# Kernel optimization log

Hardware: AMD Instinct MI355X
Metric: run time of the kernel (lower is better)

The kernel has to match this reference:

```python
import jax, jax.numpy as jnp
import numpy as np
from jax import lax

N, L, B = 256, 20, 10      # batch, max_seq (baskets), max_bas (items/basket)
D, H, ASP, K = 128, 128, 4, 16  # dim, h, aspects, nbNUM
NITEMS = 20000
H2 = 2 * H


def setup_inputs() -> dict:
    key = jax.random.key(0)
    ks = jax.random.split(key, 20)
    nrm = lambda k, shape, s=0.05: (jax.random.normal(k, shape) * s).astype(jnp.float32)
    seq = jax.random.randint(ks[0], (N, L, B), 0, NITEMS + 1)          # indices into itemEmb
    uHis = jax.random.uniform(ks[1], (N, NITEMS), dtype=jnp.float32)   # dense user history
    itemEmb = nrm(ks[2], (NITEMS + 1, D), 0.1).at[0].set(0.0)          # padding_idx=0 row zeroed
    fc1_w = nrm(ks[3], (1, L * B * D)); fc1_b = jnp.zeros((1,), jnp.float32)
    aspProju = nrm(ks[4], (ASP, 1, H))
    aspProji = nrm(ks[5], (ASP, D, H))
    dh_w = nrm(ks[6], (H, D)); dh_b = jnp.zeros((H,), jnp.float32)
    wih0 = nrm(ks[7], (4 * H2, H2)); whh0 = nrm(ks[8], (4 * H2, H2))
    bih0 = jnp.zeros((4 * H2,), jnp.float32); bhh0 = jnp.zeros((4 * H2,), jnp.float32)
    wih1 = nrm(ks[9], (4 * H2, H2)); whh1 = nrm(ks[10], (4 * H2, H2))
    bih1 = jnp.zeros((4 * H2,), jnp.float32); bhh1 = jnp.zeros((4 * H2,), jnp.float32)
    out_w = nrm(ks[11], (NITEMS, H2)); out_b = jnp.zeros((NITEMS,), jnp.float32)
    his_w = nrm(ks[12], (H2, NITEMS)); his_b = jnp.zeros((H2,), jnp.float32)
    g1_w = nrm(ks[13], (1, H2)); g1_b = jnp.zeros((1,), jnp.float32)
    g2_w = nrm(ks[14], (1, H2)); g2_b = jnp.zeros((1,), jnp.float32)
    return dict(seq=seq, uHis=uHis, itemEmb=itemEmb, fc1_w=fc1_w, fc1_b=fc1_b,
                aspProju=aspProju, aspProji=aspProji, dh_w=dh_w, dh_b=dh_b,
                wih0=wih0, whh0=whh0, bih0=bih0, bhh0=bhh0,
                wih1=wih1, whh1=whh1, bih1=bih1, bhh1=bhh1,
                out_w=out_w, out_b=out_b, his_w=his_w, his_b=his_b,
                g1_w=g1_w, g1_b=g1_b, g2_w=g2_w, g2_b=g2_b)


def _lstm_layer(x, wih, whh, bih, bhh):
    # x: [N, T, in]; PyTorch gate order i, f, g, o
    Hs = whh.shape[1]
    def step(carry, xt):
        h, c = carry
        g = xt @ wih.T + bih + h @ whh.T + bhh
        i, f, gg, o = jnp.split(g, 4, axis=-1)
        c = jax.nn.sigmoid(f) * c + jax.nn.sigmoid(i) * jnp.tanh(gg)
        h = jax.nn.sigmoid(o) * jnp.tanh(c)
        return (h, c), h
    h0 = jnp.zeros((x.shape[0], Hs), x.dtype)
    _, ys = lax.scan(step, (h0, h0), jnp.swapaxes(x, 0, 1))
    return jnp.swapaxes(ys, 0, 1)


def reference(seq, uHis, itemEmb, fc1_w, fc1_b, aspProju, aspProji, dh_w, dh_b,
              wih0, whh0, bih0, bhh0, wih1, whh1, bih1, bhh1,
              out_w, out_b, his_w, his_b, g1_w, g1_b, g2_w, g2_b):
    n, l, b = seq.shape
    embs = itemEmb[seq]                                   # [N,L,B,D]
    # MIE_user: fresh fc1 -> scalar per user, project per aspect
    u_embs = embs.reshape(n, -1) @ fc1_w.T + fc1_b        # [N,1]
    userAsp = jnp.tanh(jnp.einsum('no,aoh->nah', u_embs, aspProju))      # [N,ASP,H]
    # MIE_item
    itemAsp = jnp.tanh(jnp.einsum('nlbd,adh->nalbh', embs, aspProji))    # [N,ASP,L,B,H]
    # SNA: per-aspect exact L2 kNN over the batch (FAISS IndexFlatL2 equivalent)
    uA = jnp.transpose(jnp.tanh(userAsp), (1, 0, 2))      # [ASP,N,H] (double tanh, as in source)
    sq = jnp.sum(uA * uA, -1)                             # [ASP,N]
    dist = sq[:, :, None] + sq[:, None, :] - 2.0 * jnp.einsum('anh,amh->anm', uA, uA)
    dist = jnp.where(jnp.eye(n, dtype=bool)[None], -1.0, dist)   # self ranked first
    _, I = lax.top_k(lax.stop_gradient(-dist), K)         # [ASP,N,K] ascending distance
    I = I[:, :, 1:]                                       # drop self -> K-1 neighbors
    # sum of neighbor embeddings via multiplicity matmul (== gather+sum)
    M = jax.nn.one_hot(I, n, dtype=embs.dtype).sum(2)     # [ASP,N,N]
    nb_sum = jnp.einsum('apn,nlbd->aplbd', M, embs)       # [ASP,N,L,B,D]
    nb_h = nb_sum @ dh_w.T + dh_b                         # [ASP,N,L,B,H]
    embs_PI = jnp.transpose(nb_h.sum(axis=3), (1, 0, 2, 3))        # [N,ASP,L,H]
    embs_UI = jnp.tanh(itemAsp).sum(axis=3)               # [N,ASP,L,H] (double tanh)
    neighbAsps = jnp.concatenate([embs_UI, embs_PI], axis=-1)      # [N,ASP,L,2H]
    # raw view (not permute!) then max-pool over last dim of size ASP
    x = jnp.reshape(neighbAsps, (n, l, H2, ASP)).max(axis=-1)      # [N,L,2H]
    # 2-layer LSTM (eval mode: inter-layer dropout inactive)
    y = _lstm_layer(x, wih0, whh0, bih0, bhh0)
    y = _lstm_layer(y, wih1, whh1, bih1, bhh1)
    h_agg = jnp.tanh(y.sum(axis=1))                       # [N,2H]
    probs = jax.nn.softmax(h_agg @ out_w.T + out_b, axis=-1)       # [N,NITEMS]
    uHis_h = uHis @ his_w.T + his_b                        # [N,2H]
    gate = jax.nn.sigmoid(uHis_h @ g1_w.T + g1_b + h_agg @ g2_w.T + g2_b)  # [N,1]
    scores = gate * probs + (1.0 - gate) * uHis
    return scores
```

## Files before the change

kernel.cpp:

```cpp
#include <hip/hip_runtime.h>
#include <math.h>

#define N_ 256
#define L_ 20
#define B_ 10
#define D_ 128
#define H_ 128
#define ASP_ 4
#define KK_ 16
#define NIT_ 20000
#define H2_ 256
#define G4_ 1024
#define LBD_ 25600
#define NL_ 5120
#define NLB_ 51200

typedef __attribute__((ext_vector_type(8))) short bf16x8;
typedef __attribute__((ext_vector_type(4))) short bf16x4;
typedef __attribute__((ext_vector_type(4))) float f32x4;

__device__ __forceinline__ float sigf_fast(float x){
  return __builtin_amdgcn_rcpf(1.0f + __expf(-x));
}
__device__ __forceinline__ float tanh_fast(float x){
  return 1.0f - 2.0f*__builtin_amdgcn_rcpf(__expf(2.0f*x) + 1.0f);
}
__device__ __forceinline__ unsigned short f2b(float f){
  unsigned int u = __float_as_uint(f);
  unsigned int r = (u + 0x7FFFu + ((u>>16)&1u)) >> 16;
  return (unsigned short)r;
}
__device__ __forceinline__ float b2f(unsigned short b){
  return __uint_as_float(((unsigned int)b) << 16);
}

__global__ void k_gather(const int* __restrict__ seq, const float* __restrict__ itemEmb,
                         float* __restrict__ embs, unsigned short* __restrict__ ebh){
  int row = blockIdx.x;
  int t = threadIdx.x;
  int idx = seq[row];
  float v = itemEmb[idx*D_ + t];
  embs[row*D_ + t] = v;
  ebh[row*D_ + t] = f2b(v);
}

__global__ void k_fc1(const float* __restrict__ embs, const float* __restrict__ w,
                      const float* __restrict__ b, float* __restrict__ u){
  int n = blockIdx.x; int t = threadIdx.x;
  float s = 0.f;
  for (int i = t; i < LBD_; i += 256) s += embs[n*LBD_+i]*w[i];
  __shared__ float red[256];
  red[t]=s; __syncthreads();
  for (int o=128;o>0;o>>=1){ if(t<o) red[t]+=red[t+o]; __syncthreads(); }
  if(t==0) u[n]=red[0]+b[0];
}

__global__ void k_uasq(const float* __restrict__ u, const float* __restrict__ proju,
                       float* __restrict__ ua, float* __restrict__ sq){
  int an = blockIdx.x;
  int h = threadIdx.x;
  int a = an / N_, n = an % N_;
  float v = tanhf(tanhf(u[n]*proju[a*H_+h]));
  ua[an*H_ + h] = v;
  __shared__ float red[128];
  red[h] = v*v; __syncthreads();
  for(int o=64;o>0;o>>=1){ if(h<o) red[h]+=red[h+o]; __syncthreads(); }
  if(h==0) sq[an]=red[0];
}

__global__ __launch_bounds__(256) void k_disttopk(const float* __restrict__ ua,
    const float* __restrict__ sq, int* __restrict__ nbr){
  int n = blockIdx.x, a = blockIdx.y, m = threadIdx.x;
  __shared__ float un[H_];
  __shared__ float row[N_];
  if(m < H_) un[m] = ua[(a*N_+n)*H_ + m];
  __syncthreads();
  const float* um = &ua[(a*N_+m)*H_];
  float dot=0.f;
  for(int h=0;h<H_;h++) dot += un[h]*um[h];
  float dval = sq[a*N_+n] + sq[a*N_+m] - 2.f*dot;
  if(m==n) dval = -1.0f;
  row[m] = dval;
  __syncthreads();
  if(m < 64){
    int lane = m;
    int wid = a*N_+n;
    float v[4]; int idx[4];
    #pragma unroll
    for(int j=0;j<4;j++){ int mm = lane*4 + j; v[j] = row[mm]; idx[j] = mm; }
    for(int k=0;k<KK_;k++){
      float bv = v[0]; int bi = idx[0];
      #pragma unroll
      for(int j=1;j<4;j++)
        if(v[j] < bv || (v[j]==bv && idx[j] < bi)){ bv=v[j]; bi=idx[j]; }
      float rv = bv; int ri = bi;
      #pragma unroll
      for(int o=32;o>0;o>>=1){
        float ov = __shfl_xor(rv, o, 64);
        int   oi = __shfl_xor(ri, o, 64);
        if(ov < rv || (ov==rv && oi < ri)){ rv=ov; ri=oi; }
      }
      if((ri>>2) == lane){ v[ri&3] = 3.4e38f; idx[ri&3] = 0x7fffffff; }
      if(k>0 && lane==0) nbr[wid*(KK_-1)+(k-1)] = ri;
    }
  }
}

__global__ void k_eb(const float* __restrict__ embs, float* __restrict__ eb){
  int nl = blockIdx.x; int d = threadIdx.x;
  float s=0.f;
  const float* p = &embs[nl*B_*D_ + d];
  for(int b=0;b<B_;b++) s += p[b*D_];
  eb[nl*D_ + d] = s;
}

__global__ void k_prep(const float* __restrict__ wih0, const float* __restrict__ whh0,
                       const float* __restrict__ wih1, const float* __restrict__ whh1,
                       const float* __restrict__ bih0, const float* __restrict__ bhh0,
                       const float* __restrict__ bih1, const float* __restrict__ bhh1,
                       const float* __restrict__ proji,
                       float* __restrict__ wp0, unsigned short* __restrict__ whb0,
                       float* __restrict__ wp1, unsigned short* __restrict__ whb1,
                       float* __restrict__ bp0, float* __restrict__ bp1,
                       unsigned short* __restrict__ projb){
  int i = blockIdx.x*blockDim.x + threadIdx.x;
  if(i < 262144){
    int k=i%H2_, j=i/H2_, g=j/H2_, jj=j%H2_;
    wp0[(jj*4+g)*H2_+k] = wih0[i];
  } else if(i < 524288){
    int e=i-262144; int k=e%H2_, j=e/H2_, g=j/H2_, jj=j%H2_;
    whb0[(jj*4+g)*H2_+k] = f2b(whh0[e]);
  } else if(i < 786432){
    int e=i-524288; int k=e%H2_, j=e/H2_, g=j/H2_, jj=j%H2_;
    wp1[(jj*4+g)*H2_+k] = wih1[e];
  } else if(i < 1048576){
    int e=i-786432; int k=e%H2_, j=e/H2_, g=j/H2_, jj=j%H2_;
    whb1[(jj*4+g)*H2_+k] = f2b(whh1[e]);
  } else if(i < 1114112){
    int e=i-1048576; int h=e%H_, d=(e/H_)%D_, aa=e/(D_*H_);
    projb[(aa*H_+h)*D_+d] = f2b(proji[e]);
  } else if(i < 1115136){
    int j=i-1114112; int g=j/H2_, jj=j%H2_;
    bp0[jj*4+g] = bih0[j] + bhh0[j];
  } else if(i < 1116160){
    int j=i-1115136; int g=j/H2_, jj=j%H2_;
    bp1[jj*4+g] = bih1[j] + bhh1[j];
  }
}

__global__ __launch_bounds__(256) void k_uimm(const unsigned short* __restrict__ ebh,
                                              const unsigned short* __restrict__ projb,
                                              float* __restrict__ na){
  __shared__ char smem[53248];
  unsigned short* As = (unsigned short*)smem;
  unsigned short* Bs = (unsigned short*)(smem + 20480);
  float*          Cs = (float*)smem;

  int mb = blockIdx.x;
  int a  = blockIdx.y;
  int tid = threadIdx.x;

  const unsigned short* asrc = ebh + (size_t)mb*10240;
  #pragma unroll
  for(int t=0;t<5;t++){
    int c = tid + t*256;
    int row = c >> 4;
    *(bf16x8*)(As + 8*(c ^ (row&7))) = *(const bf16x8*)(asrc + 8*c);
  }
  const unsigned short* bsrc = projb + a*16384;
  #pragma unroll
  for(int t=0;t<8;t++){
    int c = tid + t*256;
    int row = c >> 4;
    *(bf16x8*)(Bs + 8*(c ^ (row&7))) = *(const bf16x8*)(bsrc + 8*c);
  }
  __syncthreads();

  int lane = tid & 63, wave = tid >> 6;
  int l15 = lane & 15, l4 = lane >> 4;
  f32x4 acc[5][2] = {};
  #pragma unroll
  for(int kk=0;kk<4;kk++){
    bf16x8 bfr[2];
    #pragma unroll
    for(int tc=0;tc<2;tc++){
      int h = (wave*2+tc)*16 + l15;
      int c = h*16 + kk*4 + l4;
      bfr[tc] = *(const bf16x8*)(Bs + 8*(c ^ (h&7)));
    }
    #pragma unroll
    for(int tr=0;tr<5;tr++){
      int R = tr*16 + l15;
      int c = R*16 + kk*4 + l4;
      bf16x8 afr = *(const bf16x8*)(As + 8*(c ^ (R&7)));
      acc[tr][0] = __builtin_amdgcn_mfma_f32_16x16x32_bf16(afr, bfr[0], acc[tr][0], 0,0,0);
      acc[tr][1] = __builtin_amdgcn_mfma_f32_16x16x32_bf16(afr, bfr[1], acc[tr][1], 0,0,0);
    }
  }
  __syncthreads();

  #pragma unroll
  for(int tr=0;tr<5;tr++)
    #pragma unroll
    for(int tc=0;tc<2;tc++){
      int col = (wave*2+tc)*16 + l15;
      #pragma unroll
      for(int r=0;r<4;r++){
        int R = tr*16 + l4*4 + r;
        Cs[R*128 + col] = tanh_fast(tanh_fast(acc[tr][tc][r]));
      }
    }
  __syncthreads();

  #pragma unroll
  for(int t=0;t<4;t++){
    int oi = t*256 + tid;
    int g = oi >> 7, col = oi & 127;
    float s = 0.f;
    const float* p = Cs + g*1280 + col;
    #pragma unroll
    for(int b=0;b<10;b++) s += p[b*128];
    int nl = mb*8 + g;
    int n = nl/L_, l = nl%L_;
    na[((size_t)(n*ASP_+a)*L_ + l)*H2_ + col] = s;
  }
}

__global__ __launch_bounds__(256) void k_uhismm(const float* __restrict__ U,
    const float* __restrict__ W, const float* __restrict__ bias, float* __restrict__ C){
  __shared__ unsigned short As[2048];
  __shared__ unsigned short Bs[2048];
  int tid = threadIdx.x;
  int m0 = blockIdx.y*64, n0 = blockIdx.x*64;
  int kb0 = blockIdx.z*800;
  int row = tid & 63, q = tid >> 6;
  int lane = tid & 63, wave = tid >> 6;
  int l15 = lane & 15, l4 = lane >> 4;
  int wr = (wave>>1)*32, wc = (wave&1)*32;
  f32x4 acc[2][2] = {};
  for(int s=0;s<25;s++){
    int k0 = kb0 + s*32 + q*8;
    {
      const float* pa = &U[(size_t)(m0+row)*NIT_ + k0];
      float4 a0 = *(const float4*)pa, a1 = *(const float4*)(pa+4);
      bf16x8 av;
      av[0]=f2b(a0.x); av[1]=f2b(a0.y); av[2]=f2b(a0.z); av[3]=f2b(a0.w);
      av[4]=f2b(a1.x); av[5]=f2b(a1.y); av[6]=f2b(a1.z); av[7]=f2b(a1.w);
      *(bf16x8*)(As + 8*tid) = av;
      const float* pb = &W[(size_t)(n0+row)*NIT_ + k0];
      float4 b0 = *(const float4*)pb, b1 = *(const float4*)(pb+4);
      bf16x8 bv;
      bv[0]=f2b(b0.x); bv[1]=f2b(b0.y); bv[2]=f2b(b0.z); bv[3]=f2b(b0.w);
      bv[4]=f2b(b1.x); bv[5]=f2b(b1.y); bv[6]=f2b(b1.z); bv[7]=f2b(b1.w);
      *(bf16x8*)(Bs + 8*tid) = bv;
    }
    __syncthreads();
    bf16x8 afr[2], bfr[2];
    #pragma unroll
    for(int mt=0;mt<2;mt++) afr[mt] = *(const bf16x8*)(As + 8*(l4*64 + wr + mt*16 + l15));
    #pragma unroll
    for(int nt=0;nt<2;nt++) bfr[nt] = *(const bf16x8*)(Bs + 8*(l4*64 + wc + nt*16 + l15));
    #pragma unroll
    for(int mt=0;mt<2;mt++)
      #pragma unroll
      for(int nt=0;nt<2;nt++)
        acc[mt][nt] = __builtin_amdgcn_mfma_f32_16x16x32_bf16(afr[mt], bfr[nt], acc[mt][nt], 0,0,0);
    __syncthreads();
  }
  #pragma unroll
  for(int mt=0;mt<2;mt++)
    #pragma unroll
    for(int nt=0;nt<2;nt++){
      int col = n0 + wc + nt*16 + l15;
      #pragma unroll
      for(int r=0;r<4;r++){
        int rw = m0 + wr + mt*16 + l4*4 + r;
        float v = acc[mt][nt][r];
        if(blockIdx.z==0) v += bias[col];
        atomicAdd(&C[rw*H2_ + col], v);
      }
    }
}

__global__ __launch_bounds__(256) void k_xgmm(const float* __restrict__ A_,
    const float* __restrict__ W, const float* __restrict__ bias,
    unsigned short* __restrict__ Cb){
  __shared__ unsigned short As[2048];
  __shared__ unsigned short Bs[2048];
  int tid = threadIdx.x;
  int n0 = blockIdx.x*64, m0 = blockIdx.y*64;
  int row = tid & 63, q = tid >> 6;
  int lane = tid & 63, wave = tid >> 6;
  int l15 = lane & 15, l4 = lane >> 4;
  int wr = (wave>>1)*32, wc = (wave&1)*32;
  f32x4 acc[2][2] = {};
  for(int s=0;s<8;s++){
    int k0 = s*32 + q*8;
    {
      const float* pa = &A_[(size_t)(m0+row)*H2_ + k0];
      float4 a0 = *(const float4*)pa, a1 = *(const float4*)(pa+4);
      bf16x8 av;
      av[0]=f2b(a0.x); av[1]=f2b(a0.y); av[2]=f2b(a0.z); av[3]=f2b(a0.w);
      av[4]=f2b(a1.x); av[5]=f2b(a1.y); av[6]=f2b(a1.z); av[7]=f2b(a1.w);
      *(bf16x8*)(As + 8*tid) = av;
      const float* pb = &W[(size_t)(n0+row)*H2_ + k0];
      float4 b0 = *(const float4*)pb, b1 = *(const float4*)(pb+4);
      bf16x8 bv;
      bv[0]=f2b(b0.x); bv[1]=f2b(b0.y); bv[2]=f2b(b0.z); bv[3]=f2b(b0.w);
      bv[4]=f2b(b1.x); bv[5]=f2b(b1.y); bv[6]=f2b(b1.z); bv[7]=f2b(b1.w);
      *(bf16x8*)(Bs + 8*tid) = bv;
    }
    __syncthreads();
    bf16x8 afr[2], bfr[2];
    #pragma unroll
    for(int mt=0;mt<2;mt++) afr[mt] = *(const bf16x8*)(As + 8*(l4*64 + wr + mt*16 + l15));
    #pragma unroll
    for(int nt=0;nt<2;nt++) bfr[nt] = *(const bf16x8*)(Bs + 8*(l4*64 + wc + nt*16 + l15));
    #pragma unroll
    for(int mt=0;mt<2;mt++)
      #pragma unroll
      for(int nt=0;nt<2;nt++)
        acc[mt][nt] = __builtin_amdgcn_mfma_f32_16x16x32_bf16(afr[mt], bfr[nt], acc[mt][nt], 0,0,0);
    __syncthreads();
  }
  #pragma unroll
  for(int mt=0;mt<2;mt++)
    #pragma unroll
    for(int nt=0;nt<2;nt++){
      int col = n0 + wc + nt*16 + l15;
      float bs = bias[col];
      #pragma unroll
      for(int r=0;r<4;r++){
        int rw = m0 + wr + mt*16 + l4*4 + r;
        Cb[(size_t)rw*G4_ + col] = f2b(acc[mt][nt][r] + bs);
      }
    }
}

__global__ void k_outb(const float* __restrict__ w, unsigned short* __restrict__ wb){
  int i = blockIdx.x*blockDim.x + threadIdx.x;
  const float* p = w + (size_t)i*8;
  float4 a = *(const float4*)p, b = *(const float4*)(p+4);
  bf16x8 v;
  v[0]=f2b(a.x); v[1]=f2b(a.y); v[2]=f2b(a.z); v[3]=f2b(a.w);
  v[4]=f2b(b.x); v[5]=f2b(b.y); v[6]=f2b(b.z); v[7]=f2b(b.w);
  *(bf16x8*)(wb + (size_t)i*8) = v;
}

__global__ __launch_bounds__(256) void k_logitsmm(const unsigned short* __restrict__ Ab,
    const unsigned short* __restrict__ Wb, const float* __restrict__ bias,
    float* __restrict__ C){
  int n0 = blockIdx.x*32;
  int tid = threadIdx.x;
  int lane = tid & 63, wave = tid >> 6;
  int l15 = lane & 15, l4 = lane >> 4;
  f32x4 acc[4][2] = {};
  #pragma unroll
  for(int kk=0;kk<8;kk++){
    int k0 = kk*32 + l4*8;
    bf16x8 bfr[2];
    #pragma unroll
    for(int nt=0;nt<2;nt++)
      bfr[nt] = *(const bf16x8*)(Wb + (size_t)(n0 + nt*16 + l15)*H2_ + k0);
    #pragma unroll
    for(int mt=0;mt<4;mt++){
      bf16x8 afr = *(const bf16x8*)(Ab + (size_t)(wave*64 + mt*16 + l15)*H2_ + k0);
      acc[mt][0] = __builtin_amdgcn_mfma_f32_16x16x32_bf16(afr, bfr[0], acc[mt][0], 0,0,0);
      acc[mt][1] = __builtin_amdgcn_mfma_f32_16x16x32_bf16(afr, bfr[1], acc[mt][1], 0,0,0);
    }
  }
  #pragma unroll
  for(int mt=0;mt<4;mt++)
    #pragma unroll
    for(int nt=0;nt<2;nt++){
      int col = n0 + nt*16 + l15;
      float bs = bias[col];
      #pragma unroll
      for(int r=0;r<4;r++){
        int row = wave*64 + mt*16 + l4*4 + r;
        C[(size_t)row*NIT_ + col] = acc[mt][nt][r] + bs;
      }
    }
}

__global__ __launch_bounds__(256) void k_gemm(const float* __restrict__ A, const float* __restrict__ W,
    float* __restrict__ C, const float* __restrict__ bias,
    int M, int Nn, int K, int kchunk, int atomic_mode){
  __shared__ float As[64][17];
  __shared__ float Ws[64][17];
  int tid = threadIdx.x;
  int tx = tid & 15, ty = tid >> 4;
  int m0 = blockIdx.y*64, n0 = blockIdx.x*64;
  int kb0 = blockIdx.z*kchunk;
  int kend = kb0 + kchunk; if(kend > K) kend = K;
  float acc[4][4] = {};
  int lrow = tid >> 2;
  int lc4 = (tid & 3) * 4;
  for(int kb = kb0; kb < kend; kb += 16){
    {
      int gr = m0 + lrow;
      float4 v = make_float4(0,0,0,0);
      if(gr < M) v = *(const float4*)&A[(long)gr*K + kb + lc4];
      As[lrow][lc4+0]=v.x; As[lrow][lc4+1]=v.y; As[lrow][lc4+2]=v.z; As[lrow][lc4+3]=v.w;
      int gw = n0 + lrow;
      float4 u = make_float4(0,0,0,0);
      if(gw < Nn) u = *(const float4*)&W[(long)gw*K + kb + lc4];
      Ws[lrow][lc4+0]=u.x; Ws[lrow][lc4+1]=u.y; Ws[lrow][lc4+2]=u.z; Ws[lrow][lc4+3]=u.w;
    }
    __syncthreads();
    for(int k=0;k<16;k++){
      float av[4], wv[4];
      #pragma unroll
      for(int r=0;r<4;r++) av[r]=As[ty*4+r][k];
      #pragma unroll
      for(int c=0;c<4;c++) wv[c]=Ws[tx*4+c][k];
      #pragma unroll
      for(int r=0;r<4;r++)
        #pragma unroll
        for(int c=0;c<4;c++) acc[r][c] += av[r]*wv[c];
    }
    __syncthreads();
  }
  for(int r=0;r<4;r++){
    int row = m0 + ty*4 + r; if(row >= M) continue;
    for(int c=0;c<4;c++){
      int col = n0 + tx*4 + c; if(col >= Nn) continue;
      float v = acc[r][c];
      if(bias && blockIdx.z==0) v += bias[col];
      if(atomic_mode) atomicAdd(&C[(long)row*Nn+col], v);
      else C[(long)row*Nn+col] = v;
    }
  }
}

__global__ void k_pi(const float* __restrict__ e2, const int* __restrict__ nbr,
                     const float* __restrict__ dh_b, float* __restrict__ na){
  int n = blockIdx.x, a = blockIdx.y, h = threadIdx.x;
  __shared__ int nb[KK_-1];
  if(h < KK_-1) nb[h] = nbr[(a*N_+n)*(KK_-1)+h];
  __syncthreads();
  float bias = (float)B_ * dh_b[h];
  for(int l=0;l<L_;l++){
    float s = bias;
    for(int k=0;k<KK_-1;k++) s += e2[(long)(nb[k]*L_ + l)*H_ + h];
    na[((long)(n*ASP_+a)*L_ + l)*H2_ + H_ + h] = s;
  }
}

__global__ void k_xmax(const float* __restrict__ na, float* __restrict__ x){
  int i = blockIdx.x*blockDim.x + threadIdx.x;
  if(i >= N_*L_*H2_) return;
  int n = i / (L_*H2_);
  int j = i % (L_*H2_);
  const float* p = &na[(long)n*ASP_*L_*H2_ + 4*j];
  x[i] = fmaxf(fmaxf(p[0],p[1]), fmaxf(p[2],p[3]));
}

__global__ __launch_bounds__(1024) void k_lstm_layer(
    const unsigned short* __restrict__ Whb,
    const unsigned short* __restrict__ xgb,
    float* __restrict__ Y){
  __shared__ unsigned short wc[65536];
  __shared__ unsigned short hs[2][16*H2_];
  int tid = threadIdx.x;
  int n0 = blockIdx.x * 16;
  int lane = tid & 63, wave = tid >> 6;
  int l15 = lane & 15, l4 = lane >> 4;
  int n = n0 + l15;
  float creg[4] = {0.f,0.f,0.f,0.f};
  {
    int ct0 = wave*4;
    #pragma unroll
    for(int it=0; it<8; it++){
      int c = it*64 + lane;
      int row = c >> 5;
      bf16x8 w8 = *(const bf16x8*)(Whb + (size_t)(ct0*16+row)*H2_ + (c&31)*8);
      *(bf16x8*)(wc + 8*((wave<<9) + (c ^ (row&7)))) = w8;
    }
  }
  const unsigned short* wptr[3];
  #pragma unroll
  for(int i=0;i<3;i++) wptr[i] = Whb + (size_t)((wave*4+1+i)*16 + l15)*H2_ + l4*8;
  const unsigned short* wc0 = wc + (wave<<12);
  __syncthreads();
  for(int t=0; t<L_; t++){
    bf16x4 xgv[4];
    #pragma unroll
    for(int i=0;i<4;i++){
      int jj = wave*16 + i*4 + l4;
      xgv[i] = *(const bf16x4*)(xgb + ((size_t)n*L_ + t)*G4_ + jj*4);
    }
    f32x4 acc[4] = {};
    if(t > 0){
      const unsigned short* hbuf = hs[(t+1)&1];
      bf16x8 hfr[8];
      #pragma unroll
      for(int kk=0; kk<8; kk++){
        int ch = l15*32 + kk*4 + l4;
        hfr[kk] = *(const bf16x8*)(hbuf + 8*(ch ^ (l15&7)));
      }
      #pragma unroll
      for(int kk=0; kk<8; kk++){
        bf16x8 wfr[4];
        wfr[0] = *(const bf16x8*)(wc0 + 8*((l15*32 + kk*4 + l4) ^ (l15&7)));
        #pragma unroll
        for(int i=0;i<3;i++) wfr[1+i] = *(const bf16x8*)(wptr[i] + kk*32);
        #pragma unroll
        for(int i=0;i<4;i++)
          acc[i] = __builtin_amdgcn_mfma_f32_16x16x32_bf16(wfr[i], hfr[kk], acc[i], 0,0,0);
      }
    }
    unsigned short* hout = hs[t&1];
    #pragma unroll
    for(int i=0;i<4;i++){
      int jj = wave*16 + i*4 + l4;
      float gi = acc[i][0] + b2f((unsigned short)xgv[i][0]);
      float gf = acc[i][1] + b2f((unsigned short)xgv[i][1]);
      float gg = acc[i][2] + b2f((unsigned short)xgv[i][2]);
      float go = acc[i][3] + b2f((unsigned short)xgv[i][3]);
      float cnew = sigf_fast(gf)*creg[i] + sigf_fast(gi)*tanh_fast(gg);
      creg[i] = cnew;
      float hnew = sigf_fast(go)*tanh_fast(cnew);
      Y[((size_t)n*L_ + t)*H2_ + jj] = hnew;
      int ch = l15*32 + (jj>>3);
      *(unsigned short*)((char*)hout + 16*(ch ^ (l15&7)) + (jj&7)*2) = f2b(hnew);
    }
    __syncthreads();
  }
}

__global__ void k_hagg_gate(const float* __restrict__ y1, const float* __restrict__ uhish,
                            const float* __restrict__ g1w, const float* __restrict__ g1b,
                            const float* __restrict__ g2w, const float* __restrict__ g2b,
                            float* __restrict__ hagg, unsigned short* __restrict__ haggb,
                            float* __restrict__ gate){
  int n = blockIdx.x; int jj = threadIdx.x;
  float s=0.f;
  for(int t=0;t<L_;t++) s += y1[((long)n*L_+t)*H2_ + jj];
  float v = tanhf(s);
  hagg[n*H2_+jj] = v;
  haggb[n*H2_+jj] = f2b(v);
  __shared__ float red[256];
  red[jj] = uhish[n*H2_+jj]*g1w[jj] + v*g2w[jj];
  __syncthreads();
  for(int o=128;o>0;o>>=1){ if(jj<o) red[jj]+=red[jj+o]; __syncthreads(); }
  if(jj==0) gate[n] = 1.f/(1.f+expf(-(red[0]+g1b[0]+g2b[0])));
}

__global__ __launch_bounds__(512) void k_softmax_out(const float* __restrict__ logits,
    const float* __restrict__ gate, const float* __restrict__ uHis, float* __restrict__ out){
  int n = blockIdx.x; int t = threadIdx.x;
  const float* row = &logits[(long)n*NIT_];
  float m = -3.4e38f;
  for(int i=t;i<NIT_;i+=512) m = fmaxf(m, row[i]);
  __shared__ float red[512];
  __shared__ float mm, ss;
  red[t]=m; __syncthreads();
  for(int o=256;o>0;o>>=1){ if(t<o) red[t]=fmaxf(red[t],red[t+o]); __syncthreads(); }
  if(t==0) mm = red[0];
  __syncthreads();
  float s=0.f;
  for(int i=t;i<NIT_;i+=512) s += __expf(row[i]-mm);
  __syncthreads();
  red[t]=s; __syncthreads();
  for(int o=256;o>0;o>>=1){ if(t<o) red[t]+=red[t+o]; __syncthreads(); }
  if(t==0) ss = red[0];
  __syncthreads();
  float g = gate[n];
  float* orow = out + (long)n*NIT_;
  const float* urow = uHis + (long)n*NIT_;
  for(int i=t;i<NIT_;i+=512){
    float p = __expf(row[i]-mm)/ss;
    orow[i] = g*p + (1.f-g)*urow[i];
  }
}

extern "C" void kernel_launch(void* const* d_in, const int* in_sizes, int n_in,
                              void* d_out, int out_size, void* d_ws, size_t ws_size,
                              hipStream_t stream) {
  const int*   seq     = (const int*)  d_in[0];
  const float* uHis    = (const float*)d_in[1];
  const float* itemEmb = (const float*)d_in[2];
  const float* fc1_w   = (const float*)d_in[3];
  const float* fc1_b   = (const float*)d_in[4];
  const float* aspProju= (const float*)d_in[5];
  const float* aspProji= (const float*)d_in[6];
  const float* dh_w    = (const float*)d_in[7];
  const float* dh_b    = (const float*)d_in[8];
  const float* wih0    = (const float*)d_in[9];
  const float* whh0    = (const float*)d_in[10];
  const float* bih0    = (const float*)d_in[11];
  const float* bhh0    = (const float*)d_in[12];
  const float* wih1    = (const float*)d_in[13];
  const float* whh1    = (const float*)d_in[14];
  const float* bih1    = (const float*)d_in[15];
  const float* bhh1    = (const float*)d_in[16];
  const float* out_w   = (const float*)d_in[17];
  const float* out_b   = (const float*)d_in[18];
  const float* his_w   = (const float*)d_in[19];
  const float* his_b   = (const float*)d_in[20];
  const float* g1_w    = (const float*)d_in[21];
  const float* g1_b    = (const float*)d_in[22];
  const float* g2_w    = (const float*)d_in[23];
  const float* g2_b    = (const float*)d_in[24];

  float* ws = (float*)d_ws;
  float* embs = ws + 0;
  float* cub  = ws + 6553600;
  float* na   = ws + 13107200;
  float* x    = ws + 18350080;
  float* y0   = ws + 19660800;
  float* y1   = ws + 20971520;
  float* eb   = ws + 22282240;
  float* e2   = ws + 22937600;
  float* ua   = ws + 23855104;
  float* projT= ws + 23986176;
  float* wp0  = ws + 24051712;
  float* whp0 = ws + 24313856;
  float* wp1  = ws + 24576000;
  float* whp1 = ws + 24838144;
  float* bp0  = ws + 25100288;
  float* bp1  = ws + 25101312;
  float* uemb = ws + 25167872;
  float* sqb  = ws + 25168128;
  int*   nbr  = (int*)(ws + 25169152);
  float* uhish= ws + 25184512;
  float* hagg = ws + 25250048;
  float* gateb =ws + 25316096;
  float* logits = embs;
  unsigned short* ebh   = (unsigned short*)cub;
  unsigned short* xgb   = (unsigned short*)cub;
  unsigned short* projb = (unsigned short*)projT;
  unsigned short* outwb = (unsigned short*)na;
  unsigned short* haggb = (unsigned short*)x;
  unsigned short* whb0  = (unsigned short*)whp0;
  unsigned short* whb1  = (unsigned short*)whp1;

  k_gather<<<NLB_, D_, 0, stream>>>(seq, itemEmb, embs, ebh);
  k_fc1<<<N_, 256, 0, stream>>>(embs, fc1_w, fc1_b, uemb);
  k_uasq<<<ASP_*N_, 128, 0, stream>>>(uemb, aspProju, ua, sqb);
  k_disttopk<<<dim3(N_,ASP_), 256, 0, stream>>>(ua, sqb, nbr);
  k_eb<<<NL_, D_, 0, stream>>>(embs, eb);
  k_gemm<<<dim3(2, 80, 1), 256, 0, stream>>>(eb, dh_w, e2, nullptr, NL_, H_, D_, D_, 0);
  k_prep<<<4360, 256, 0, stream>>>(wih0, whh0, wih1, whh1, bih0, bhh0, bih1, bhh1,
                                   aspProji, wp0, whb0, wp1, whb1, bp0, bp1, projb);
  k_uimm<<<dim3(NL_/8, ASP_), 256, 0, stream>>>(ebh, projb, na);
  k_pi<<<dim3(N_,ASP_), H_, 0, stream>>>(e2, nbr, dh_b, na);
  k_xmax<<<(N_*L_*H2_+255)/256, 256, 0, stream>>>(na, x);
  k_outb<<<2500, 256, 0, stream>>>(out_w, outwb);
  k_xgmm<<<dim3(16,80), 256, 0, stream>>>(x, wp0, bp0, xgb);
  k_lstm_layer<<<16, 1024, 0, stream>>>(whb0, xgb, y0);
  k_xgmm<<<dim3(16,80), 256, 0, stream>>>(y0, wp1, bp1, xgb);
  k_lstm_layer<<<16, 1024, 0, stream>>>(whb1, xgb, y1);
  hipMemsetAsync(uhish, 0, N_*H2_*sizeof(float), stream);
  k_uhismm<<<dim3(4,4,25), 256, 0, stream>>>(uHis, his_w, his_b, uhish);
  k_hagg_gate<<<N_, 256, 0, stream>>>(y1, uhish, g1_w, g1_b, g2_w, g2_b, hagg, haggb, gateb);
  k_logitsmm<<<625, 256, 0, stream>>>(haggb, outwb, out_b, logits);
  k_softmax_out<<<N_, 512, 0, stream>>>(logits, gateb, uHis, (float*)d_out);
}
```

Measured before the change: 522.4 us.

## Fuse gather with basket sum, convert out_w in GEMM, cache softmax exps in LDS

The embedding gather now also accumulates the per-basket sum, which removes the separate k_eb pass that re-read embs. The standalone out_w fp32-to-bf16 conversion kernel is dropped, and k_logitsmm reads fp32 weights and converts them in registers. This avoids one extra write and read of a bf16 copy but doubles the weight bytes the GEMM loads. The softmax kernel keeps the exponentials in a 80KB LDS buffer instead of re-reading logits and recomputing exp, which raises LDS use per block and may limit occupancy.

```diff
diff --git a/kernel.cpp b/kernel.cpp
--- a/kernel.cpp
+++ b/kernel.cpp
@@ -34,14 +34,21 @@
   return __uint_as_float(((unsigned int)b) << 16);
 }
 
-__global__ void k_gather(const int* __restrict__ seq, const float* __restrict__ itemEmb,
-                         float* __restrict__ embs, unsigned short* __restrict__ ebh){
-  int row = blockIdx.x;
-  int t = threadIdx.x;
-  int idx = seq[row];
-  float v = itemEmb[idx*D_ + t];
-  embs[row*D_ + t] = v;
-  ebh[row*D_ + t] = f2b(v);
+__global__ void k_gather2(const int* __restrict__ seq, const float* __restrict__ itemEmb,
+                          float* __restrict__ embs, unsigned short* __restrict__ ebh,
+                          float* __restrict__ eb){
+  int nl = blockIdx.x;
+  int d = threadIdx.x;
+  float s = 0.f;
+  #pragma unroll
+  for(int b=0;b<B_;b++){
+    int idx = seq[nl*B_ + b];
+    float v = itemEmb[(size_t)idx*D_ + d];
+    embs[(size_t)(nl*B_+b)*D_ + d] = v;
+    ebh[(size_t)(nl*B_+b)*D_ + d] = f2b(v);
+    s += v;
+  }
+  eb[(size_t)nl*D_ + d] = s;
 }
 
 __global__ void k_fc1(const float* __restrict__ embs, const float* __restrict__ w,
@@ -104,14 +111,6 @@
       if(k>0 && lane==0) nbr[wid*(KK_-1)+(k-1)] = ri;
     }
   }
-}
-
-__global__ void k_eb(const float* __restrict__ embs, float* __restrict__ eb){
-  int nl = blockIdx.x; int d = threadIdx.x;
-  float s=0.f;
-  const float* p = &embs[nl*B_*D_ + d];
-  for(int b=0;b<B_;b++) s += p[b*D_];
-  eb[nl*D_ + d] = s;
 }
 
 __global__ void k_prep(const float* __restrict__ wih0, const float* __restrict__ whh0,
@@ -337,18 +336,8 @@
     }
 }
 
-__global__ void k_outb(const float* __restrict__ w, unsigned short* __restrict__ wb){
-  int i = blockIdx.x*blockDim.x + threadIdx.x;
-  const float* p = w + (size_t)i*8;
-  float4 a = *(const float4*)p, b = *(const float4*)(p+4);
-  bf16x8 v;
-  v[0]=f2b(a.x); v[1]=f2b(a.y); v[2]=f2b(a.z); v[3]=f2b(a.w);
-  v[4]=f2b(b.x); v[5]=f2b(b.y); v[6]=f2b(b.z); v[7]=f2b(b.w);
-  *(bf16x8*)(wb + (size_t)i*8) = v;
-}
-
 __global__ __launch_bounds__(256) void k_logitsmm(const unsigned short* __restrict__ Ab,
-    const unsigned short* __restrict__ Wb, const float* __restrict__ bias,
+    const float* __restrict__ Wf, const float* __restrict__ bias,
     float* __restrict__ C){
   int n0 = blockIdx.x*32;
   int tid = threadIdx.x;
@@ -360,8 +349,14 @@
     int k0 = kk*32 + l4*8;
     bf16x8 bfr[2];
     #pragma unroll
-    for(int nt=0;nt<2;nt++)
-      bfr[nt] = *(const bf16x8*)(Wb + (size_t)(n0 + nt*16 + l15)*H2_ + k0);
+    for(int nt=0;nt<2;nt++){
+      const float* pb = &Wf[(size_t)(n0 + nt*16 + l15)*H2_ + k0];
+      float4 b0 = *(const float4*)pb, b1 = *(const float4*)(pb+4);
+      bf16x8 bv;
+      bv[0]=f2b(b0.x); bv[1]=f2b(b0.y); bv[2]=f2b(b0.z); bv[3]=f2b(b0.w);
+      bv[4]=f2b(b1.x); bv[5]=f2b(b1.y); bv[6]=f2b(b1.z); bv[7]=f2b(b1.w);
+      bfr[nt] = bv;
+    }
     #pragma unroll
     for(int mt=0;mt<4;mt++){
       bf16x8 afr = *(const bf16x8*)(Ab + (size_t)(wave*64 + mt*16 + l15)*H2_ + k0);
@@ -549,18 +544,23 @@
 
 __global__ __launch_bounds__(512) void k_softmax_out(const float* __restrict__ logits,
     const float* __restrict__ gate, const float* __restrict__ uHis, float* __restrict__ out){
+  __shared__ float pe[NIT_];
+  __shared__ float red[512];
+  __shared__ float mm, ss;
   int n = blockIdx.x; int t = threadIdx.x;
   const float* row = &logits[(long)n*NIT_];
   float m = -3.4e38f;
   for(int i=t;i<NIT_;i+=512) m = fmaxf(m, row[i]);
-  __shared__ float red[512];
-  __shared__ float mm, ss;
   red[t]=m; __syncthreads();
   for(int o=256;o>0;o>>=1){ if(t<o) red[t]=fmaxf(red[t],red[t+o]); __syncthreads(); }
   if(t==0) mm = red[0];
   __syncthreads();
   float s=0.f;
-  for(int i=t;i<NIT_;i+=512) s += __expf(row[i]-mm);
+  for(int i=t;i<NIT_;i+=512){
+    float e = __expf(row[i]-mm);
+    pe[i] = e;
+    s += e;
+  }
   __syncthreads();
   red[t]=s; __syncthreads();
   for(int o=256;o>0;o>>=1){ if(t<o) red[t]+=red[t+o]; __syncthreads(); }
@@ -570,7 +570,7 @@
   float* orow = out + (long)n*NIT_;
   const float* urow = uHis + (long)n*NIT_;
   for(int i=t;i<NIT_;i+=512){
-    float p = __expf(row[i]-mm)/ss;
+    float p = pe[i]/ss;
     orow[i] = g*p + (1.f-g)*urow[i];
   }
 }
@@ -631,23 +631,20 @@
   unsigned short* ebh   = (unsigned short*)cub;
   unsigned short* xgb   = (unsigned short*)cub;
   unsigned short* projb = (unsigned short*)projT;
-  unsigned short* outwb = (unsigned short*)na;
   unsigned short* haggb = (unsigned short*)x;
   unsigned short* whb0  = (unsigned short*)whp0;
   unsigned short* whb1  = (unsigned short*)whp1;
 
-  k_gather<<<NLB_, D_, 0, stream>>>(seq, itemEmb, embs, ebh);
+  k_gather2<<<NL_, D_, 0, stream>>>(seq, itemEmb, embs, ebh, eb);
   k_fc1<<<N_, 256, 0, stream>>>(embs, fc1_w, fc1_b, uemb);
   k_uasq<<<ASP_*N_, 128, 0, stream>>>(uemb, aspProju, ua, sqb);
   k_disttopk<<<dim3(N_,ASP_), 256, 0, stream>>>(ua, sqb, nbr);
-  k_eb<<<NL_, D_, 0, stream>>>(embs, eb);
   k_gemm<<<dim3(2, 80, 1), 256, 0, stream>>>(eb, dh_w, e2, nullptr, NL_, H_, D_, D_, 0);
   k_prep<<<4360, 256, 0, stream>>>(wih0, whh0, wih1, whh1, bih0, bhh0, bih1, bhh1,
                                    aspProji, wp0, whb0, wp1, whb1, bp0, bp1, projb);
   k_uimm<<<dim3(NL_/8, ASP_), 256, 0, stream>>>(ebh, projb, na);
   k_pi<<<dim3(N_,ASP_), H_, 0, stream>>>(e2, nbr, dh_b, na);
   k_xmax<<<(N_*L_*H2_+255)/256, 256, 0, stream>>>(na, x);
-  k_outb<<<2500, 256, 0, stream>>>(out_w, outwb);
   k_xgmm<<<dim3(16,80), 256, 0, stream>>>(x, wp0, bp0, xgb);
   k_lstm_layer<<<16, 1024, 0, stream>>>(whb0, xgb, y0);
   k_xgmm<<<dim3(16,80), 256, 0, stream>>>(y0, wp1, bp1, xgb);
@@ -655,6 +652,6 @@
   hipMemsetAsync(uhish, 0, N_*H2_*sizeof(float), stream);
   k_uhismm<<<dim3(4,4,25), 256, 0, stream>>>(uHis, his_w, his_b, uhish);
   k_hagg_gate<<<N_, 256, 0, stream>>>(y1, uhish, g1_w, g1_b, g2_w, g2_b, hagg, haggb, gateb);
-  k_logitsmm<<<625, 256, 0, stream>>>(haggb, outwb, out_b, logits);
+  k_logitsmm<<<625, 256, 0, stream>>>(haggb, out_w, out_b, logits);
   k_softmax_out<<<N_, 512, 0, stream>>>(logits, gateb, uHis, (float*)d_out);
 }
```

Result: faster. 500.1 us (-4.3%).
